# Optimization experiments

Hardware: AMD Instinct MI355X
Metric: run time of the kernel (lower is better)

## Reference

```python
import jax, jax.numpy as jnp
import numpy as np

WEIGHT_BITS = 5
QUANT_BITS = 16
BN_EPS = 1e-5


def _quant_weight_pow2(w):
    # Round weights to signed powers of two; exponent clipped per DeepShift:
    # shift range = [-(2^(bits-1)-2), 0] = [-14, 0] for 5-bit weights.
    shift_min = -(2 ** (WEIGHT_BITS - 1) - 2)
    sign = jnp.sign(w)
    p = jnp.clip(jnp.round(jnp.log2(jnp.abs(w) + 1e-20)), shift_min, 0.0)
    wq = sign * jnp.exp2(p)
    # straight-through estimator
    return w + jax.lax.stop_gradient(wq - w)


def _quant_act(x):
    # Symmetric per-tensor linear quantization to QUANT_BITS (16-bit) with STE.
    qmax = 2.0 ** (QUANT_BITS - 1) - 1.0
    scale = jnp.maximum(jnp.max(jnp.abs(x)), 1e-12) / qmax
    xq = jnp.round(x / scale) * scale
    return x + jax.lax.stop_gradient(xq - x)


def _conv(x, w, stride=1, pad=0, groups=1):
    return jax.lax.conv_general_dilated(
        x, w, (stride, stride), [(pad, pad), (pad, pad)],
        dimension_numbers=("NCHW", "OIHW", "NCHW"),
        feature_group_count=groups)


def _shift_conv(x, w, stride=1, pad=0, groups=1, bias=None):
    y = _conv(_quant_act(x), _quant_weight_pow2(w), stride, pad, groups)
    if bias is not None:
        y = y + bias[None, :, None, None]
    return y


def _bn(x, g, b, m, v):
    inv = g * jax.lax.rsqrt(v + BN_EPS)
    return x * inv[None, :, None, None] + (b - m * inv)[None, :, None, None]


def setup_inputs() -> dict:
    key = jax.random.key(0)
    ks = jax.random.split(key, 8)
    B, C_in, H, W = 32, 1024, 32, 32
    width, C_out = 256, 1024
    inp = {
        "x": jax.random.normal(ks[0], (B, C_in, H, W), jnp.float32),
        "w1": jax.random.normal(ks[1], (width, C_in, 1, 1), jnp.float32) * 0.05,
        "peg_w": jax.random.normal(ks[2], (width, 1, 3, 3), jnp.float32) * 0.1,
        "peg_b": jax.random.normal(ks[3], (width,), jnp.float32) * 0.01,
        "w2": jax.random.normal(ks[4], (width, width, 3, 3), jnp.float32) * 0.05,
        "w3": jax.random.normal(ks[5], (C_out, width, 1, 1), jnp.float32) * 0.05,
        "bn1_g": jax.random.uniform(ks[6], (width,), jnp.float32, 0.5, 1.5),
        "bn1_b": jnp.zeros((width,), jnp.float32),
        "bn1_m": jnp.zeros((width,), jnp.float32),
        "bn1_v": jnp.ones((width,), jnp.float32),
        "bn2_g": jax.random.uniform(ks[7], (width,), jnp.float32, 0.5, 1.5),
        "bn2_b": jnp.zeros((width,), jnp.float32),
        "bn2_m": jnp.zeros((width,), jnp.float32),
        "bn2_v": jnp.ones((width,), jnp.float32),
        "bn3_g": jax.random.uniform(jax.random.fold_in(key, 9), (C_out,), jnp.float32, 0.5, 1.5),
        "bn3_b": jnp.zeros((C_out,), jnp.float32),
        "bn3_m": jnp.zeros((C_out,), jnp.float32),
        "bn3_v": jnp.ones((C_out,), jnp.float32),
    }
    return inp


def reference(x, w1, peg_w, peg_b, w2, w3,
              bn1_g, bn1_b, bn1_m, bn1_v,
              bn2_g, bn2_b, bn2_m, bn2_v,
              bn3_g, bn3_b, bn3_m, bn3_v):
    residual = x  # downsample is Identity (inplanes == outplanes, stride == 1)
    h = _shift_conv(x, w1)                                   # 1x1 1024->256
    h = _shift_conv(h, peg_w, stride=1, pad=1, groups=256,
                    bias=peg_b)                               # depthwise 3x3 PEG
    h = jax.nn.relu(_bn(h, bn1_g, bn1_b, bn1_m, bn1_v))
    h = _shift_conv(h, w2, stride=1, pad=1)                   # 3x3 256->256
    h = jax.nn.relu(_bn(h, bn2_g, bn2_b, bn2_m, bn2_v))
    h = _shift_conv(h, w3)                                    # 1x1 256->1024
    h = _bn(h, bn3_g, bn3_b, bn3_m, bn3_v)
    return jax.nn.relu(h + residual)
```

## Files before the change

### kernel.cpp

```cpp
#include <hip/hip_runtime.h>

typedef _Float16 f16;
typedef _Float16 f16x8 __attribute__((ext_vector_type(8)));
typedef float f32x4 __attribute__((ext_vector_type(4)));
typedef unsigned short u16;
typedef unsigned int u32;
typedef u32 u32x4 __attribute__((ext_vector_type(4)));

#define WS_BN1_INV  256u
#define WS_BN1_BETA 1280u
#define WS_BN2_INV  2304u
#define WS_BN2_BETA 3328u
#define WS_BN3_INV  4352u
#define WS_BN3_BETA 8448u
#define WS_PEG_B    12544u
#define WS_PEGQ     13568u
#define WS_W1Q      18432u
#define WS_W3Q      542720u
#define WS_W2Q      1067008u
#define WS_H1T      2246656u
#define WS_H2T      19023872u


__device__ __forceinline__ int badf(float f){
  union { float f; u32 u; } c; c.f = f;
  return (c.u & 0x7f800000u) == 0x7f800000u;
}
__device__ __forceinline__ float qpow2(float w){
  float a = fabsf(w) + 1e-20f;
  float p = rintf(log2f(a));
  p = fminf(fmaxf(p, -14.0f), 0.0f);
  float m = exp2f(p);
  return (w > 0.0f) ? m : ((w < 0.0f) ? -m : 0.0f);
}
__device__ __forceinline__ u32 pack2(float a, float b){
  union { f16 h[2]; u32 u; } p; p.h[0] = (f16)a; p.h[1] = (f16)b; return p.u;
}
#define SWZ(row, slot) ((((slot) ^ ((row) >> 1) ^ ((row) >> 3))) & 3)

__device__ __forceinline__ void mfma_step(const char* lds, int wm, int wn,
                                          int lr, int lg, f32x4 acc[4][4]){
  f16x8 a[4], bb[4];
  #pragma unroll
  for (int mf = 0; mf < 4; ++mf){
    int row = (wm << 6) + (mf << 4) + lr;
    a[mf] = *(const f16x8*)(lds + (row << 6) + (SWZ(row, lg) << 4));
  }
  #pragma unroll
  for (int nf = 0; nf < 4; ++nf){
    int row = (wn << 6) + (nf << 4) + lr;
    bb[nf] = *(const f16x8*)(lds + 8192 + (row << 6) + (SWZ(row, lg) << 4));
  }
  #pragma unroll
  for (int mf = 0; mf < 4; ++mf)
    #pragma unroll
    for (int nf = 0; nf < 4; ++nf)
      acc[mf][nf] = __builtin_amdgcn_mfma_f32_16x16x32_f16(a[mf], bb[nf], acc[mf][nf], 0, 0, 0);
}

__global__ __launch_bounds__(256) void prep_kernel(
    const float* __restrict__ w1, const float* __restrict__ pegw, const float* __restrict__ pegb,
    const float* __restrict__ w2, const float* __restrict__ w3,
    const float* g1, const float* b1, const float* m1, const float* v1,
    const float* g2, const float* b2, const float* m2, const float* v2,
    const float* g3, const float* b3, const float* m3, const float* v3,
    char* ws){
  int i = blockIdx.x * 256 + threadIdx.x;
  if (i < 262144){ ((f16*)(ws + WS_W1Q))[i] = (f16)qpow2(w1[i]); return; }
  i -= 262144;
  if (i < 589824){
    int tap = i >> 16, rem = i & 65535;
    int co = rem >> 8, ci = rem & 255;
    ((f16*)(ws + WS_W2Q))[i] = (f16)qpow2(w2[(((co << 8) + ci) * 9) + tap]);
    return;
  }
  i -= 589824;
  if (i < 262144){ ((f16*)(ws + WS_W3Q))[i] = (f16)qpow2(w3[i]); return; }
  i -= 262144;
  if (i < 2304){
    int tap = i >> 8, c = i & 255;
    ((f16*)(ws + WS_PEGQ))[i] = (f16)qpow2(pegw[c * 9 + tap]);
    return;
  }
  i -= 2304;
  if (i < 256){ ((float*)(ws + WS_PEG_B))[i] = pegb[i]; return; }
  i -= 256;
  if (i < 256){
    float inv = g1[i] / sqrtf(v1[i] + 1e-5f);
    ((float*)(ws + WS_BN1_INV))[i] = inv;
    ((float*)(ws + WS_BN1_BETA))[i] = b1[i] - m1[i] * inv;
    return;
  }
  i -= 256;
  if (i < 256){
    float inv = g2[i] / sqrtf(v2[i] + 1e-5f);
    ((float*)(ws + WS_BN2_INV))[i] = inv;
    ((float*)(ws + WS_BN2_BETA))[i] = b2[i] - m2[i] * inv;
    return;
  }
  i -= 256;
  if (i < 1024){
    float inv = g3[i] / sqrtf(v3[i] + 1e-5f);
    ((float*)(ws + WS_BN3_INV))[i] = inv;
    ((float*)(ws + WS_BN3_BETA))[i] = b3[i] - m3[i] * inv;
  }
}

__global__ __launch_bounds__(512) void conv1_kernel(const float* __restrict__ x, char* ws){
  __shared__ __align__(16) char lds[49152];
  const f16* w1q = (const f16*)(ws + WS_W1Q);
  f16* h1T = (f16*)(ws + WS_H1T);

  int tid = threadIdx.x, bid = blockIdx.x;
  int b = bid >> 3, m0 = (bid & 7) << 7;
  int l = tid & 63, wid = tid >> 6, wm = wid >> 2, wn = wid & 3;
  int lr = l & 15, lg = l >> 4;
  f32x4 acc[4][4] = {};

  int q = tid & 31;
  int c = tid >> 5;
  const float* xb = x + (((size_t)(b << 10)) << 10) + m0 + (q << 2);
  int aslot = c >> 2, aoff = (c & 3) << 2;

  f32x4 d0, d1; u32x4 wb0, wb1;
  {
    const float* src = xb + (((size_t)(c << 1)) << 10);
    d0 = *(const f32x4*)src;
    d1 = *(const f32x4*)(src + 1024);
    int s0 = tid, r0 = s0 >> 2, sl0 = s0 & 3;
    int s1 = tid + 512, r1 = s1 >> 2, sl1 = s1 & 3;
    wb0 = *(const u32x4*)(w1q + ((size_t)r0 << 10) + (sl0 << 3));
    wb1 = *(const u32x4*)(w1q + ((size_t)r1 << 10) + (sl1 << 3));
  }
  {
    char* A = lds;
    #pragma unroll
    for (int j = 0; j < 4; ++j){
      int row = (q << 2) + j;
      *(u32*)(A + (row << 6) + (SWZ(row, aslot) << 4) + aoff) = pack2(d0[j], d1[j]);
    }
    int s0 = tid, r0 = s0 >> 2, sl0 = s0 & 3;
    int s1 = tid + 512, r1 = s1 >> 2, sl1 = s1 & 3;
    *(u32x4*)(lds + 8192 + (r0 << 6) + (SWZ(r0, sl0) << 4)) = wb0;
    *(u32x4*)(lds + 8192 + (r1 << 6) + (SWZ(r1, sl1) << 4)) = wb1;
  }
  __syncthreads();

  for (int ks = 0; ks < 32; ++ks){
    const char* cur = lds + ((ks & 1) ? 24576 : 0);
    char* nxt = lds + ((ks & 1) ? 0 : 24576);
    if (ks < 31){
      int k0 = (ks + 1) << 5;
      const float* src = xb + (((size_t)(k0 + (c << 1))) << 10);
      d0 = *(const f32x4*)src;
      d1 = *(const f32x4*)(src + 1024);
      int s0 = tid, r0 = s0 >> 2, sl0 = s0 & 3;
      int s1 = tid + 512, r1 = s1 >> 2, sl1 = s1 & 3;
      wb0 = *(const u32x4*)(w1q + ((size_t)r0 << 10) + k0 + (sl0 << 3));
      wb1 = *(const u32x4*)(w1q + ((size_t)r1 << 10) + k0 + (sl1 << 3));
    }
    f16x8 a[4], bb[4];
    #pragma unroll
    for (int mf = 0; mf < 4; ++mf){
      int row = (wm << 6) + (mf << 4) + lr;
      a[mf] = *(const f16x8*)(cur + (row << 6) + (SWZ(row, lg) << 4));
    }
    #pragma unroll
    for (int nf = 0; nf < 4; ++nf){
      int row = (wn << 6) + (nf << 4) + lr;
      bb[nf] = *(const f16x8*)(cur + 8192 + (row << 6) + (SWZ(row, lg) << 4));
    }
    #pragma unroll
    for (int mf = 0; mf < 4; ++mf)
      #pragma unroll
      for (int nf = 0; nf < 4; ++nf)
        acc[mf][nf] = __builtin_amdgcn_mfma_f32_16x16x32_f16(a[mf], bb[nf], acc[mf][nf], 0, 0, 0);
    if (ks < 31){
      #pragma unroll
      for (int j = 0; j < 4; ++j){
        int row = (q << 2) + j;
        *(u32*)(nxt + (row << 6) + (SWZ(row, aslot) << 4) + aoff) = pack2(d0[j], d1[j]);
      }
      int s0 = tid, r0 = s0 >> 2, sl0 = s0 & 3;
      int s1 = tid + 512, r1 = s1 >> 2, sl1 = s1 & 3;
      *(u32x4*)(nxt + 8192 + (r0 << 6) + (SWZ(r0, sl0) << 4)) = wb0;
      *(u32x4*)(nxt + 8192 + (r1 << 6) + (SWZ(r1, sl1) << 4)) = wb1;
    }
    __syncthreads();
  }

  #pragma unroll
  for (int mf = 0; mf < 4; ++mf){
    int p0 = m0 + (wm << 6) + (mf << 4) + (lg << 2);
    size_t base = ((size_t)(b << 10) + p0) << 8;
    #pragma unroll
    for (int nf = 0; nf < 4; ++nf){
      int co = (wn << 6) + (nf << 4) + lr;
      #pragma unroll
      for (int r = 0; r < 4; ++r)
        h1T[base + ((size_t)r << 8) + co] = (f16)acc[mf][nf][r];
    }
  }
}

__global__ __launch_bounds__(256) void peg_kernel(char* ws){
  __shared__ __align__(16) f16 tile[3][32][256];
  const f16* h1T = (const f16*)(ws + WS_H1T);
  const f16* pegq = (const f16*)(ws + WS_PEGQ);
  const float* pb  = (const float*)(ws + WS_PEG_B);
  const float* inv1 = (const float*)(ws + WS_BN1_INV);
  const float* bt1  = (const float*)(ws + WS_BN1_BETA);
  f16* h2T = (f16*)(ws + WS_H2T);

  int tid = threadIdx.x;
  int b = blockIdx.x >> 5, h = blockIdx.x & 31;

  #pragma unroll
  for (int r = 0; r < 3; ++r){
    int hh = h + r - 1;
    #pragma unroll
    for (int i = 0; i < 4; ++i){
      int chunk = tid + (i << 8);
      int px = chunk >> 5, cg = chunk & 31;
      u32x4 d = {0u, 0u, 0u, 0u};
      if ((u32)hh < 32u)
        d = *(const u32x4*)(h1T + (((size_t)(b << 10) + (hh << 5) + px) << 8) + (cg << 3));
      *(u32x4*)(&tile[r][px][cg << 3]) = d;
    }
  }
  __syncthreads();

  int c0 = (tid & 31) << 3;
  int q  = tid >> 5;
  float acc[4][8];
  #pragma unroll
  for (int i = 0; i < 4; ++i)
    #pragma unroll
    for (int j = 0; j < 8; ++j) acc[i][j] = pb[c0 + j];

  #pragma unroll
  for (int ky = 0; ky < 3; ++ky){
    #pragma unroll
    for (int kx = 0; kx < 3; ++kx){
      f16x8 wv = *(const f16x8*)(pegq + ((ky * 3 + kx) << 8) + c0);
      #pragma unroll
      for (int i = 0; i < 4; ++i){
        int ww = (q << 2) + i + kx - 1;
        if ((u32)ww < 32u){
          f16x8 v = *(const f16x8*)(&tile[ky][ww][c0]);
          #pragma unroll
          for (int j = 0; j < 8; ++j) acc[i][j] += (float)v[j] * (float)wv[j];
        }
      }
    }
  }

  f32x4 iv0 = *(const f32x4*)(inv1 + c0), iv1 = *(const f32x4*)(inv1 + c0 + 4);
  f32x4 bt0 = *(const f32x4*)(bt1 + c0),  bt1v = *(const f32x4*)(bt1 + c0 + 4);
  #pragma unroll
  for (int i = 0; i < 4; ++i){
    f16x8 o;
    #pragma unroll
    for (int j = 0; j < 8; ++j){
      float ivj = (j < 4) ? iv0[j] : iv1[j - 4];
      float btj = (j < 4) ? bt0[j] : bt1v[j - 4];
      o[j] = (f16)fmaxf(acc[i][j] * ivj + btj, 0.0f);
    }
    int p = (h << 5) + (q << 2) + i;
    *(f16x8*)(h2T + (((size_t)(b << 10) + p) << 8) + c0) = o;
  }
}

__global__ __launch_bounds__(512) void conv2_kernel(char* ws){
  __shared__ __align__(16) char lds[104448 + 32768];
  const f16* h2T = (const f16*)(ws + WS_H2T);
  const f16* w2q = (const f16*)(ws + WS_W2Q);
  const float* inv2 = (const float*)(ws + WS_BN2_INV);
  const float* bt2  = (const float*)(ws + WS_BN2_BETA);
  f16* h3T = (f16*)(ws + WS_H1T);

  int tid = threadIdx.x, bid = blockIdx.x;
  int b = bid >> 3, mt = bid & 7;
  int h0 = mt << 2;
  int m0 = mt << 7;
  int l = tid & 63, wid = tid >> 6, wm = wid >> 2, wn = wid & 3;
  int lr = l & 15, lg = l >> 4;
  char* A = lds;
  char* B0 = lds + 104448;
  char* B1 = lds + 104448 + 16384;

  for (int chunk = tid; chunk < 6528; chunk += 512){
    int r = chunk / 1088;
    int rem = chunk - r * 1088;
    int cc = rem >> 5, slot = rem & 31;
    int hh = h0 - 1 + r, wwp = cc - 1;
    u32x4 d = {0u, 0u, 0u, 0u};
    if ((u32)hh < 32u && (u32)wwp < 32u)
      d = *(const u32x4*)(h2T + (((size_t)(b << 10) + (hh << 5) + wwp) << 8) + (slot << 3));
    int sw = slot ^ ((cc & 7) << 2);
    *(u32x4*)(A + ((r * 34 + cc) << 9) + (sw << 4)) = d;
  }
  #pragma unroll
  for (int i = 0; i < 2; ++i){
    int chunk = tid + (i << 9);
    int co = chunk >> 2, slot = chunk & 3;
    u32x4 d = *(const u32x4*)(w2q + (co << 8) + (slot << 3));
    *(u32x4*)(B0 + (co << 6) + (SWZ(co, slot) << 4)) = d;
  }
  __syncthreads();

  f32x4 acc[4][4] = {};
  for (int tap = 0; tap < 9; ++tap){
    int dy = tap / 3 - 1, dx = tap % 3 - 1;
    int rowbase[4], key[4];
    #pragma unroll
    for (int mf = 0; mf < 4; ++mf){
      int p = (wm << 6) + (mf << 4) + lr;
      int rr = (p >> 5) + dy + 1;
      int cc = (p & 31) + dx + 1;
      rowbase[mf] = ((rr * 34 + cc) << 9) + (lg << 4);
      key[mf] = cc & 7;
    }
    #pragma unroll 2
    for (int ks = 0; ks < 8; ++ks){
      int t = (tap << 3) + ks;
      u32x4 st[2];
      int have = (t < 71);
      int t1 = t + 1, wtap = t1 >> 3, wks = t1 & 7;
      const f16* srcb = w2q + wtap * 65536 + (wks << 5);
      if (have){
        #pragma unroll
        for (int i = 0; i < 2; ++i){
          int chunk = tid + (i << 9);
          int co = chunk >> 2, slot = chunk & 3;
          st[i] = *(const u32x4*)(srcb + (co << 8) + (slot << 3));
        }
      }
      const char* bs = (t & 1) ? B1 : B0;
      f16x8 a[4], bb[4];
      #pragma unroll
      for (int mf = 0; mf < 4; ++mf)
        a[mf] = *(const f16x8*)(A + rowbase[mf] + ((ks ^ key[mf]) << 6));
      #pragma unroll
      for (int nf = 0; nf < 4; ++nf){
        int row = (wn << 6) + (nf << 4) + lr;
        bb[nf] = *(const f16x8*)(bs + (row << 6) + (SWZ(row, lg) << 4));
      }
      #pragma unroll
      for (int mf = 0; mf < 4; ++mf)
        #pragma unroll
        for (int nf = 0; nf < 4; ++nf)
          acc[mf][nf] = __builtin_amdgcn_mfma_f32_16x16x32_f16(a[mf], bb[nf], acc[mf][nf], 0, 0, 0);
      if (have){
        char* bd = (t1 & 1) ? B1 : B0;
        #pragma unroll
        for (int i = 0; i < 2; ++i){
          int chunk = tid + (i << 9);
          int co = chunk >> 2, slot = chunk & 3;
          *(u32x4*)(bd + (co << 6) + (SWZ(co, slot) << 4)) = st[i];
        }
      }
      __syncthreads();
    }
  }

  #pragma unroll
  for (int mf = 0; mf < 4; ++mf){
    int p0 = m0 + (wm << 6) + (mf << 4) + (lg << 2);
    size_t base = ((size_t)(b << 10) + p0) << 8;
    #pragma unroll
    for (int nf = 0; nf < 4; ++nf){
      int co = (wn << 6) + (nf << 4) + lr;
      float iv = inv2[co], bt = bt2[co];
      #pragma unroll
      for (int r = 0; r < 4; ++r)
        h3T[base + ((size_t)r << 8) + co] = (f16)fmaxf(acc[mf][nf][r] * iv + bt, 0.0f);
    }
  }
}

__global__ __launch_bounds__(256) void conv3_kernel(const float* __restrict__ x,
                                                    float* __restrict__ out, char* ws){
  __shared__ __align__(16) char lds[16384];
  const f16* w3q = (const f16*)(ws + WS_W3Q);
  const f16* h3T = (const f16*)(ws + WS_H1T);
  const float* inv3 = (const float*)(ws + WS_BN3_INV);
  const float* bt3  = (const float*)(ws + WS_BN3_BETA);

  int tid = threadIdx.x, bid = blockIdx.x;
  int b = bid >> 6, m0 = ((bid >> 3) & 7) << 7, n0 = (bid & 7) << 7;
  int l = tid & 63, wid = tid >> 6, wm = wid >> 1, wn = wid & 1;
  int lr = l & 15, lg = l >> 4;
  f32x4 acc[4][4] = {};

  for (int ks = 0; ks < 8; ++ks){
    int k0 = ks << 5;
    #pragma unroll
    for (int i = 0; i < 2; ++i){
      int s = tid + (i << 8);
      int row = s >> 2, slot = s & 3;
      u32x4 dA = *(const u32x4*)(w3q + ((size_t)(m0 + row) << 8) + k0 + (slot << 3));
      u32x4 dB = *(const u32x4*)(h3T + (((size_t)(b << 10) + n0 + row) << 8) + k0 + (slot << 3));
      *(u32x4*)(lds + (row << 6) + (SWZ(row, slot) << 4)) = dA;
      *(u32x4*)(lds + 8192 + (row << 6) + (SWZ(row, slot) << 4)) = dB;
    }
    __syncthreads();
    mfma_step(lds, wm, wn, lr, lg, acc);
    __syncthreads();
  }

  #pragma unroll
  for (int mf = 0; mf < 4; ++mf){
    int co0 = m0 + (wm << 6) + (mf << 4) + (lg << 2);
    f32x4 iv = *(const f32x4*)(inv3 + co0);
    f32x4 bt = *(const f32x4*)(bt3 + co0);
    #pragma unroll
    for (int nf = 0; nf < 4; ++nf){
      int p = n0 + (wn << 6) + (nf << 4) + lr;
      #pragma unroll
      for (int r = 0; r < 4; ++r){
        size_t idx = (((size_t)(b << 10) + co0 + r) << 10) + p;
        float z = acc[mf][nf][r] * iv[r] + bt[r] + x[idx];
        float rr = fmaxf(z, 0.0f);
        if (badf(z)) rr = 512.0f;
        out[idx] = rr;
      }
    }
  }
}

extern "C" void kernel_launch(void* const* d_in, const int* in_sizes, int n_in,
                              void* d_out, int out_size, void* d_ws, size_t ws_size,
                              hipStream_t stream){
  const float* x    = (const float*)d_in[0];
  const float* w1   = (const float*)d_in[1];
  const float* pegw = (const float*)d_in[2];
  const float* pegb = (const float*)d_in[3];
  const float* w2   = (const float*)d_in[4];
  const float* w3   = (const float*)d_in[5];
  const float* g1 = (const float*)d_in[6];
  const float* b1 = (const float*)d_in[7];
  const float* m1 = (const float*)d_in[8];
  const float* v1 = (const float*)d_in[9];
  const float* g2 = (const float*)d_in[10];
  const float* b2 = (const float*)d_in[11];
  const float* m2 = (const float*)d_in[12];
  const float* v2 = (const float*)d_in[13];
  const float* g3 = (const float*)d_in[14];
  const float* b3 = (const float*)d_in[15];
  const float* m3 = (const float*)d_in[16];
  const float* v3 = (const float*)d_in[17];
  char* ws = (char*)d_ws;

  prep_kernel<<<4368, 256, 0, stream>>>(w1, pegw, pegb, w2, w3,
                                        g1, b1, m1, v1, g2, b2, m2, v2,
                                        g3, b3, m3, v3, ws);
  conv1_kernel<<<256, 512, 0, stream>>>(x, ws);
  peg_kernel<<<1024, 256, 0, stream>>>(ws);
  conv2_kernel<<<256, 512, 0, stream>>>(ws);
  conv3_kernel<<<2048, 256, 0, stream>>>(x, (float*)d_out, ws);
}
```

Baseline: 177.4 us.

## Fuse 3x3 conv2 and 1x1 conv3 into one kernel via LDS-resident tile

The conv2 and conv3 kernels are merged into one. The conv2 output tile (128 pixels x 256 channels, fp16) stays in shared memory instead of being written to global memory as h3T and read back. The fused kernel then loops over 8 output-channel tiles of w3, loading each 128x256 weight tile into LDS and running MFMAs with the BN3, residual and ReLU epilogue. This removes the h3T round trip and one launch, but conv3 now runs on only 256 blocks of 512 threads with large LDS use, so there is less parallelism than the previous 2048-block launch.

```diff
diff --git a/kernel.cpp b/kernel.cpp
--- a/kernel.cpp
+++ b/kernel.cpp
@@ -37,26 +37,6 @@
   union { f16 h[2]; u32 u; } p; p.h[0] = (f16)a; p.h[1] = (f16)b; return p.u;
 }
 #define SWZ(row, slot) ((((slot) ^ ((row) >> 1) ^ ((row) >> 3))) & 3)
-
-__device__ __forceinline__ void mfma_step(const char* lds, int wm, int wn,
-                                          int lr, int lg, f32x4 acc[4][4]){
-  f16x8 a[4], bb[4];
-  #pragma unroll
-  for (int mf = 0; mf < 4; ++mf){
-    int row = (wm << 6) + (mf << 4) + lr;
-    a[mf] = *(const f16x8*)(lds + (row << 6) + (SWZ(row, lg) << 4));
-  }
-  #pragma unroll
-  for (int nf = 0; nf < 4; ++nf){
-    int row = (wn << 6) + (nf << 4) + lr;
-    bb[nf] = *(const f16x8*)(lds + 8192 + (row << 6) + (SWZ(row, lg) << 4));
-  }
-  #pragma unroll
-  for (int mf = 0; mf < 4; ++mf)
-    #pragma unroll
-    for (int nf = 0; nf < 4; ++nf)
-      acc[mf][nf] = __builtin_amdgcn_mfma_f32_16x16x32_f16(a[mf], bb[nf], acc[mf][nf], 0, 0, 0);
-}
 
 __global__ __launch_bounds__(256) void prep_kernel(
     const float* __restrict__ w1, const float* __restrict__ pegw, const float* __restrict__ pegb,
@@ -271,13 +251,16 @@
   }
 }
 
-__global__ __launch_bounds__(512) void conv2_kernel(char* ws){
-  __shared__ __align__(16) char lds[104448 + 32768];
+__global__ __launch_bounds__(512) void conv23_kernel(const float* __restrict__ x,
+                                                     float* __restrict__ out, char* ws){
+  __shared__ __align__(16) char lds[137216];
   const f16* h2T = (const f16*)(ws + WS_H2T);
   const f16* w2q = (const f16*)(ws + WS_W2Q);
+  const f16* w3q = (const f16*)(ws + WS_W3Q);
   const float* inv2 = (const float*)(ws + WS_BN2_INV);
   const float* bt2  = (const float*)(ws + WS_BN2_BETA);
-  f16* h3T = (f16*)(ws + WS_H1T);
+  const float* inv3 = (const float*)(ws + WS_BN3_INV);
+  const float* bt3  = (const float*)(ws + WS_BN3_BETA);
 
   int tid = threadIdx.x, bid = blockIdx.x;
   int b = bid >> 3, mt = bid & 7;
@@ -366,66 +349,81 @@
 
   #pragma unroll
   for (int mf = 0; mf < 4; ++mf){
-    int p0 = m0 + (wm << 6) + (mf << 4) + (lg << 2);
-    size_t base = ((size_t)(b << 10) + p0) << 8;
     #pragma unroll
     for (int nf = 0; nf < 4; ++nf){
-      int co = (wn << 6) + (nf << 4) + lr;
-      float iv = inv2[co], bt = bt2[co];
-      #pragma unroll
-      for (int r = 0; r < 4; ++r)
-        h3T[base + ((size_t)r << 8) + co] = (f16)fmaxf(acc[mf][nf][r] * iv + bt, 0.0f);
-    }
-  }
-}
-
-__global__ __launch_bounds__(256) void conv3_kernel(const float* __restrict__ x,
-                                                    float* __restrict__ out, char* ws){
-  __shared__ __align__(16) char lds[16384];
-  const f16* w3q = (const f16*)(ws + WS_W3Q);
-  const f16* h3T = (const f16*)(ws + WS_H1T);
-  const float* inv3 = (const float*)(ws + WS_BN3_INV);
-  const float* bt3  = (const float*)(ws + WS_BN3_BETA);
-
-  int tid = threadIdx.x, bid = blockIdx.x;
-  int b = bid >> 6, m0 = ((bid >> 3) & 7) << 7, n0 = (bid & 7) << 7;
-  int l = tid & 63, wid = tid >> 6, wm = wid >> 1, wn = wid & 1;
-  int lr = l & 15, lg = l >> 4;
-  f32x4 acc[4][4] = {};
-
-  for (int ks = 0; ks < 8; ++ks){
-    int k0 = ks << 5;
-    #pragma unroll
-    for (int i = 0; i < 2; ++i){
-      int s = tid + (i << 8);
-      int row = s >> 2, slot = s & 3;
-      u32x4 dA = *(const u32x4*)(w3q + ((size_t)(m0 + row) << 8) + k0 + (slot << 3));
-      u32x4 dB = *(const u32x4*)(h3T + (((size_t)(b << 10) + n0 + row) << 8) + k0 + (slot << 3));
-      *(u32x4*)(lds + (row << 6) + (SWZ(row, slot) << 4)) = dA;
-      *(u32x4*)(lds + 8192 + (row << 6) + (SWZ(row, slot) << 4)) = dB;
+      int c = (wn << 6) + (nf << 4) + lr;
+      float iv = inv2[c], bt = bt2[c];
+      int slot = c >> 3, off = (c & 7) << 1;
+      #pragma unroll
+      for (int r = 0; r < 4; ++r){
+        int px = (wm << 6) + (mf << 4) + (lg << 2) + r;
+        float f = fmaxf(acc[mf][nf][r] * iv + bt, 0.0f);
+        *(f16*)(lds + (px << 9) + ((slot ^ ((px & 7) << 2)) << 4) + off) = (f16)f;
+      }
+    }
+  }
+  __syncthreads();
+
+  for (int cot = 0; cot < 8; ++cot){
+    #pragma unroll
+    for (int i = 0; i < 8; ++i){
+      int s = tid + (i << 9);
+      int row = s >> 5, slot = s & 31;
+      u32x4 d = *(const u32x4*)(w3q + (((size_t)(cot << 7) + row) << 8) + (slot << 3));
+      *(u32x4*)(lds + 65536 + (row << 9) + ((slot ^ ((row & 7) << 2)) << 4)) = d;
     }
     __syncthreads();
-    mfma_step(lds, wm, wn, lr, lg, acc);
+
+    f32x4 acc2[4][2] = {};
+    #pragma unroll
+    for (int ks = 0; ks < 8; ++ks){
+      f16x8 a[4], bb[2];
+      #pragma unroll
+      for (int mf = 0; mf < 4; ++mf){
+        int row = (wm << 6) + (mf << 4) + lr;
+        int slot = (ks << 2) | lg;
+        a[mf] = *(const f16x8*)(lds + 65536 + (row << 9) + ((slot ^ ((row & 7) << 2)) << 4));
+      }
+      #pragma unroll
+      for (int nf = 0; nf < 2; ++nf){
+        int row = (wn << 5) + (nf << 4) + lr;
+        int slot = (ks << 2) | lg;
+        bb[nf] = *(const f16x8*)(lds + (row << 9) + ((slot ^ ((row & 7) << 2)) << 4));
+      }
+      #pragma unroll
+      for (int mf = 0; mf < 4; ++mf)
+        #pragma unroll
+        for (int nf = 0; nf < 2; ++nf)
+          acc2[mf][nf] = __builtin_amdgcn_mfma_f32_16x16x32_f16(a[mf], bb[nf], acc2[mf][nf], 0, 0, 0);
+    }
+
+    #pragma unroll
+    for (int mf = 0; mf < 4; ++mf){
+      int co0 = (cot << 7) + (wm << 6) + (mf << 4) + (lg << 2);
+      f32x4 iv = *(const f32x4*)(inv3 + co0);
+      f32x4 bt = *(const f32x4*)(bt3 + co0);
+      float xr[8];
+      #pragma unroll
+      for (int nf = 0; nf < 2; ++nf){
+        int px = (wn << 5) + (nf << 4) + lr;
+        #pragma unroll
+        for (int r = 0; r < 4; ++r)
+          xr[(nf << 2) + r] = x[(((size_t)(b << 10) + co0 + r) << 10) + m0 + px];
+      }
+      #pragma unroll
+      for (int nf = 0; nf < 2; ++nf){
+        int px = (wn << 5) + (nf << 4) + lr;
+        #pragma unroll
+        for (int r = 0; r < 4; ++r){
+          size_t idx = (((size_t)(b << 10) + co0 + r) << 10) + m0 + px;
+          float z = acc2[mf][nf][r] * iv[r] + bt[r] + xr[(nf << 2) + r];
+          float rr = fmaxf(z, 0.0f);
+          if (badf(z)) rr = 512.0f;
+          out[idx] = rr;
+        }
+      }
+    }
     __syncthreads();
-  }
-
-  #pragma unroll
-  for (int mf = 0; mf < 4; ++mf){
-    int co0 = m0 + (wm << 6) + (mf << 4) + (lg << 2);
-    f32x4 iv = *(const f32x4*)(inv3 + co0);
-    f32x4 bt = *(const f32x4*)(bt3 + co0);
-    #pragma unroll
-    for (int nf = 0; nf < 4; ++nf){
-      int p = n0 + (wn << 6) + (nf << 4) + lr;
-      #pragma unroll
-      for (int r = 0; r < 4; ++r){
-        size_t idx = (((size_t)(b << 10) + co0 + r) << 10) + p;
-        float z = acc[mf][nf][r] * iv[r] + bt[r] + x[idx];
-        float rr = fmaxf(z, 0.0f);
-        if (badf(z)) rr = 512.0f;
-        out[idx] = rr;
-      }
-    }
   }
 }
 
@@ -457,6 +455,5 @@
                                         g3, b3, m3, v3, ws);
   conv1_kernel<<<256, 512, 0, stream>>>(x, ws);
   peg_kernel<<<1024, 256, 0, stream>>>(ws);
-  conv2_kernel<<<256, 512, 0, stream>>>(ws);
-  conv3_kernel<<<2048, 256, 0, stream>>>(x, (float*)d_out, ws);
-}
+  conv23_kernel<<<256, 512, 0, stream>>>(x, (float*)d_out, ws);
+}
```

After: 169.7 us. 1.05x faster.
